# Kernel tuning notes

Measured on AMD Instinct MI355X. Metric: run time of the kernel, lower is better.

The kernel has to match this reference:

```python
import jax, jax.numpy as jnp
import numpy as np

D_MODEL = 1024
D_FF = 4096
N_HEADS = 16
D_HEAD = D_MODEL // N_HEADS
CHUNK = 64
N_HASHES = 2
N_BUCKETS = 32
EPS = 1e-5


def layer_norm(x, g, b):
    mu = jnp.mean(x, axis=-1, keepdims=True)
    var = jnp.mean(jnp.square(x - mu), axis=-1, keepdims=True)
    return (x - mu) / jnp.sqrt(var + EPS) * g + b


def look_one_back(a):
    # a: [B, H, n_chunks, chunk, ...]; concat each chunk with its predecessor
    prev = jnp.roll(a, 1, axis=2)
    return jnp.concatenate([a, prev], axis=3)


def lsh_attention(x, mask, Wqk, Wv, Wo, rot):
    # x: [B, T, D]; mask: [B, T] bool (True = valid token); shared-QK LSH attention
    B, T, D = x.shape
    H, dh, nh, nb = N_HEADS, D_HEAD, N_HASHES, N_BUCKETS
    qk = (x @ Wqk).reshape(B, T, H, dh).transpose(0, 2, 1, 3)  # [B,H,T,dh]
    v = (x @ Wv).reshape(B, T, H, dh).transpose(0, 2, 1, 3)

    # --- hashing: random rotations, argmax over +/- projections ---
    rotated = jnp.einsum('bhtd,dnr->bhtnr', qk, rot)            # [B,H,T,nh,nb/2]
    rotated = jnp.concatenate([rotated, -rotated], axis=-1)     # [B,H,T,nh,nb]
    buckets = jnp.argmax(rotated, axis=-1)                      # [B,H,T,nh]
    buckets = buckets + jnp.arange(nh) * nb                     # disjoint ids per round
    buckets = buckets.transpose(0, 1, 3, 2).reshape(B, H, nh * T)

    # --- stable bucket sort ---
    total = nh * T
    pos = jnp.arange(total) % T
    sort_key = buckets * T + pos
    sticker = jnp.argsort(sort_key, axis=-1)                    # [B,H,total]
    undo = jnp.argsort(sticker, axis=-1)
    st = sticker % T                                            # original positions

    gather = lambda a: jnp.take_along_axis(a, st[..., None], axis=2)
    sqk = gather(qk)                                            # [B,H,total,dh]
    sv = gather(v)
    smask = jnp.take_along_axis(jnp.broadcast_to(mask[:, None, :], (B, H, T)), st, axis=2)

    # --- chunked local attention with one look-back chunk ---
    nch = total // CHUNK
    bq = sqk.reshape(B, H, nch, CHUNK, dh)
    bk = bq / (jnp.linalg.norm(bq, axis=-1, keepdims=True) + 1e-9)  # shared-QK: normalized keys
    bv = sv.reshape(B, H, nch, CHUNK, dh)
    bt = st.reshape(B, H, nch, CHUNK)
    bm = smask.reshape(B, H, nch, CHUNK)

    bk2 = look_one_back(bk)                                     # [B,H,nch,2*CHUNK,dh]
    bv2 = look_one_back(bv)
    bt2 = look_one_back(bt)
    bm2 = look_one_back(bm)

    dots = jnp.einsum('bhcie,bhcje->bhcij', bq, bk2) * (dh ** -0.5)
    self_mask = bt[..., :, None] == bt2[..., None, :]           # token vs itself (soft mask)
    dots = jnp.where(self_mask, -1e5, dots)
    dots = jnp.where(bm2[..., None, :], dots, -1e9)             # padding keys

    lse = jax.nn.logsumexp(dots, axis=-1, keepdims=True)
    probs = jnp.exp(dots - lse)
    bo = jnp.einsum('bhcij,bhcje->bhcie', probs, bv2)

    # --- unsort and combine hash rounds by logsumexp weights ---
    so = bo.reshape(B, H, total, dh)
    slog = lse.reshape(B, H, total, 1)
    o = jnp.take_along_axis(so, undo[..., None], axis=2).reshape(B, H, nh, T, dh)
    logits = jnp.take_along_axis(slog, undo[..., None], axis=2).reshape(B, H, nh, T, 1)
    w = jax.nn.softmax(logits, axis=2)
    out = jnp.sum(o * w, axis=2)                                # [B,H,T,dh]
    out = out.transpose(0, 2, 1, 3).reshape(B, T, D)
    return out @ Wo


def setup_inputs() -> dict:
    key = jax.random.key(0)
    ks = jax.random.split(key, 10)
    B, T = 2, 2048
    s = 0.02
    return {
        'x': jax.random.normal(ks[0], (B, T, D_MODEL), jnp.float32),
        'attn_mask': jnp.ones((B, T), bool),
        'ln1_g': jnp.ones((D_MODEL,), jnp.float32),
        'ln1_b': jnp.zeros((D_MODEL,), jnp.float32),
        'ln2_g': jnp.ones((D_MODEL,), jnp.float32),
        'ln2_b': jnp.zeros((D_MODEL,), jnp.float32),
        'Wqk': jax.random.normal(ks[1], (D_MODEL, D_MODEL), jnp.float32) * s,
        'Wv': jax.random.normal(ks[2], (D_MODEL, D_MODEL), jnp.float32) * s,
        'Wo': jax.random.normal(ks[3], (D_MODEL, D_MODEL), jnp.float32) * s,
        'rot': jax.random.normal(ks[4], (D_HEAD, N_HASHES, N_BUCKETS // 2), jnp.float32),
        'W1': jax.random.normal(ks[5], (D_MODEL, D_FF), jnp.float32) * s,
        'b1': jnp.zeros((D_FF,), jnp.float32),
        'W2': jax.random.normal(ks[6], (D_FF, D_MODEL), jnp.float32) * s,
        'b2': jnp.zeros((D_MODEL,), jnp.float32),
    }


def reference(x, attn_mask, ln1_g, ln1_b, ln2_g, ln2_b, Wqk, Wv, Wo, rot, W1, b1, W2, b2):
    # pre-norm -> LSH self-attention -> residual
    q = layer_norm(x, ln1_g, ln1_b)
    x = x + lsh_attention(q, attn_mask, Wqk, Wv, Wo, rot)
    # pre-norm -> FFN (linear-relu-linear) -> residual
    h = layer_norm(x, ln2_g, ln2_b)
    f = jax.nn.relu(h @ W1 + b1) @ W2 + b2
    return x + f
```

## Files before the change

kernel.cpp:

```cpp
#include <hip/hip_runtime.h>

typedef unsigned short u16;
typedef unsigned int u32;
typedef unsigned long long u64;
typedef __attribute__((ext_vector_type(8))) __bf16 bf16x8;
typedef __attribute__((ext_vector_type(8))) _Float16 f16x8;
typedef __attribute__((ext_vector_type(4))) float f32x4;

#define DEVI __device__ __forceinline__

DEVI float bf2f(u16 u) { u32 x = ((u32)u) << 16; return __uint_as_float(x); }
DEVI u16 f2bf(float f) {
  u32 u = __float_as_uint(f);
  return (u16)((u + 0x7FFFu + ((u >> 16) & 1u)) >> 16);
}
DEVI u16 h_bits(_Float16 h) { return __builtin_bit_cast(u16, h); }
DEVI void gload_lds16(const void* g, void* l) {
  __builtin_amdgcn_global_load_lds((const __attribute__((address_space(1))) void*)g,
                                   (__attribute__((address_space(3))) void*)l, 16, 0, 0);
}
DEVI void swz_block(int& bx, int& by) {
  int gx = gridDim.x;
  int nwg = gx * gridDim.y;
  int wg = blockIdx.y * gx + blockIdx.x;
  int q = nwg >> 3, rr = nwg & 7, xcd = wg & 7, idx = wg >> 3;
  int s = (xcd < rr ? xcd * (q + 1) : rr * (q + 1) + (xcd - rr) * q) + idx;
  bx = s % gx;
  by = s / gx;
}

__global__ __launch_bounds__(256) void transpose_k(const float* __restrict__ in,
                                                   u16* __restrict__ out, int R, int C) {
  __shared__ float tile[32][33];
  int c0 = blockIdx.x * 32, r0 = blockIdx.y * 32;
  int tx = threadIdx.x, ty = threadIdx.y;
#pragma unroll
  for (int k = 0; k < 4; k++)
    tile[ty + 8 * k][tx] = in[(size_t)(r0 + ty + 8 * k) * C + c0 + tx];
  __syncthreads();
#pragma unroll
  for (int k = 0; k < 4; k++) {
    float v = tile[tx][ty + 8 * k];
    out[(size_t)(c0 + ty + 8 * k) * R + r0 + tx] = f2bf(v);
  }
}

__global__ __launch_bounds__(256) void ln_kernel(const float* __restrict__ x,
                                                 const float* __restrict__ g,
                                                 const float* __restrict__ b,
                                                 u16* __restrict__ obf,
                                                 u16* __restrict__ oh,
                                                 u16* __restrict__ ol) {
  int row = blockIdx.x;
  const float* xr = x + (size_t)row * 1024;
  float vals[4];
  float s = 0.f, s2 = 0.f;
#pragma unroll
  for (int i = 0; i < 4; i++) {
    float v = xr[threadIdx.x + i * 256];
    vals[i] = v; s += v; s2 += v * v;
  }
#pragma unroll
  for (int off = 32; off > 0; off >>= 1) {
    s += __shfl_down(s, off);
    s2 += __shfl_down(s2, off);
  }
  __shared__ float red[8];
  int wid = threadIdx.x >> 6;
  if ((threadIdx.x & 63) == 0) { red[wid] = s; red[4 + wid] = s2; }
  __syncthreads();
  if (threadIdx.x == 0) {
    float a = red[0] + red[1] + red[2] + red[3];
    float a2 = red[4] + red[5] + red[6] + red[7];
    float mu = a * (1.0f / 1024.0f);
    red[0] = mu;
    red[1] = a2 * (1.0f / 1024.0f) - mu * mu;
  }
  __syncthreads();
  float mu = red[0];
  float inv = 1.0f / sqrtf(red[1] + 1e-5f);
#pragma unroll
  for (int i = 0; i < 4; i++) {
    int c = threadIdx.x + i * 256;
    float y = (vals[i] - mu) * inv * g[c] + b[c];
    if (obf) obf[(size_t)row * 1024 + c] = f2bf(y);
    if (oh) {
      _Float16 hh = (_Float16)y;
      _Float16 ll = (_Float16)(y - (float)hh);
      oh[(size_t)row * 1024 + c] = h_bits(hh);
      ol[(size_t)row * 1024 + c] = h_bits(ll);
    }
  }
}

__global__ __launch_bounds__(256) void w2r_kernel(const float* __restrict__ wqk,
                                                  const float* __restrict__ rot,
                                                  u16* __restrict__ w2rh,
                                                  u16* __restrict__ w2rl) {
  int idx = blockIdx.x * 256 + threadIdx.x;
  int n = idx >> 10, c = idx & 1023;
  int h = n >> 5, rj = n & 31;
  const float* wp = wqk + (size_t)c * 1024 + h * 64;
  double acc = 0.0;
  for (int d = 0; d < 64; d++) acc += (double)wp[d] * (double)rot[d * 32 + rj];
  _Float16 hh = (_Float16)acc;
  _Float16 ll = (_Float16)(acc - (double)hh);
  w2rh[idx] = h_bits(hh);
  w2rl[idx] = h_bits(ll);
}

__global__ __launch_bounds__(256) void gemm_rot_split(const u16* __restrict__ Ah,
                                                      const u16* __restrict__ Al,
                                                      const u16* __restrict__ Bh,
                                                      const u16* __restrict__ Bl,
                                                      float* __restrict__ C) {
  __shared__ __align__(16) u16 Ash[128 * 32];
  __shared__ __align__(16) u16 Asl[128 * 32];
  __shared__ __align__(16) u16 Bsh[64 * 32];
  __shared__ __align__(16) u16 Bsl[64 * 32];
  int tid = threadIdx.x;
  int bx, by;
  swz_block(bx, by);
  int m0 = by * 128, n0 = bx * 64;
  int w = tid >> 6, l = tid & 63, lr = l & 15, g = l >> 4;
  int wm = w >> 1, wn = w & 1;
  f32x4 acc[4][2];
#pragma unroll
  for (int i = 0; i < 4; i++)
#pragma unroll
    for (int j = 0; j < 2; j++) { f32x4 z = {0.f, 0.f, 0.f, 0.f}; acc[i][j] = z; }
  for (int k0 = 0; k0 < 1024; k0 += 32) {
    __syncthreads();
#pragma unroll
    for (int e = 0; e < 2; e++) {
      int idx = e * 256 + tid;
      const u16* ga = Ah + (size_t)(m0 + (idx >> 2)) * 1024 + k0 + (idx & 3) * 8;
      gload_lds16(ga, &Ash[(e * 256 + w * 64) * 8]);
      const u16* gl = Al + (size_t)(m0 + (idx >> 2)) * 1024 + k0 + (idx & 3) * 8;
      gload_lds16(gl, &Asl[(e * 256 + w * 64) * 8]);
    }
    {
      const u16* gb = Bh + (size_t)(n0 + (tid >> 2)) * 1024 + k0 + (tid & 3) * 8;
      gload_lds16(gb, &Bsh[(w * 64) * 8]);
      const u16* gb2 = Bl + (size_t)(n0 + (tid >> 2)) * 1024 + k0 + (tid & 3) * 8;
      gload_lds16(gb2, &Bsl[(w * 64) * 8]);
    }
    __syncthreads();
    f16x8 ah[4], al[4], bh[2], bl[2];
#pragma unroll
    for (int mt = 0; mt < 4; mt++) {
      ah[mt] = *(const f16x8*)&Ash[(wm * 64 + mt * 16 + lr) * 32 + g * 8];
      al[mt] = *(const f16x8*)&Asl[(wm * 64 + mt * 16 + lr) * 32 + g * 8];
    }
#pragma unroll
    for (int nt = 0; nt < 2; nt++) {
      bh[nt] = *(const f16x8*)&Bsh[(wn * 32 + nt * 16 + lr) * 32 + g * 8];
      bl[nt] = *(const f16x8*)&Bsl[(wn * 32 + nt * 16 + lr) * 32 + g * 8];
    }
#pragma unroll
    for (int mt = 0; mt < 4; mt++)
#pragma unroll
      for (int nt = 0; nt < 2; nt++) {
        acc[mt][nt] = __builtin_amdgcn_mfma_f32_16x16x32_f16(ah[mt], bh[nt], acc[mt][nt], 0, 0, 0);
        acc[mt][nt] = __builtin_amdgcn_mfma_f32_16x16x32_f16(ah[mt], bl[nt], acc[mt][nt], 0, 0, 0);
        acc[mt][nt] = __builtin_amdgcn_mfma_f32_16x16x32_f16(al[mt], bh[nt], acc[mt][nt], 0, 0, 0);
      }
  }
#pragma unroll
  for (int mt = 0; mt < 4; mt++)
#pragma unroll
    for (int nt = 0; nt < 2; nt++)
#pragma unroll
      for (int r = 0; r < 4; r++) {
        int row = m0 + wm * 64 + mt * 16 + g * 4 + r;
        int col = n0 + wn * 32 + nt * 16 + lr;
        C[(size_t)row * 512 + col] = acc[mt][nt][r];
      }
}

__global__ __launch_bounds__(256) void bucket_kernel(const float* __restrict__ rotated,
                                                     int* __restrict__ buckets) {
  int gid = blockIdx.x * 256 + threadIdx.x;
  int bh = gid >> 12;
  int rem = gid & 4095;
  int r = rem >> 11, t = rem & 2047;
  int b = bh >> 4, h = bh & 15;
  const float* rp = rotated + (size_t)(b * 2048 + t) * 512 + h * 32 + r * 16;
  float v16[16];
#pragma unroll
  for (int j = 0; j < 16; j++) v16[j] = rp[j];
  float bv = v16[0];
  int bi = 0;
#pragma unroll
  for (int jj = 1; jj < 32; jj++) {
    float v = (jj < 16) ? v16[jj] : -v16[jj - 16];
    if (v > bv) { bv = v; bi = jj; }
  }
  buckets[bh * 4096 + r * 2048 + t] = bi + r * 32;
}

__global__ __launch_bounds__(256) void sort_kernel(const int* __restrict__ buckets,
                                                   int* __restrict__ st,
                                                   int* __restrict__ undo) {
  int bh = blockIdx.x;
  __shared__ unsigned char bk[4096];
  __shared__ unsigned char rnk[4096];
  __shared__ int cnt[64 * 64];
  __shared__ int base[64];
  int tid = threadIdx.x;
  int w = tid >> 6, lane = tid & 63;
  for (int i = tid; i < 4096; i += 256) bk[i] = (unsigned char)buckets[bh * 4096 + i];
  for (int i = tid; i < 4096; i += 256) cnt[i] = 0;
  __syncthreads();
  u64 lmask = (lane == 63) ? 0x7FFFFFFFFFFFFFFFull : ((1ull << lane) - 1ull);
#pragma unroll
  for (int it = 0; it < 16; ++it) {
    int c = w * 16 + it;
    int i = c * 64 + lane;
    int b = bk[i];
    u64 m = ~0ull;
#pragma unroll
    for (int k = 0; k < 6; k++) {
      u64 bal = __ballot((b >> k) & 1);
      m &= ((b >> k) & 1) ? bal : ~bal;
    }
    int r = __popcll(m & lmask);
    rnk[i] = (unsigned char)r;
    if (r == 0) cnt[c * 64 + b] = __popcll(m);
  }
  __syncthreads();
  if (tid < 64) {
    int acc = 0;
    for (int c = 0; c < 64; c++) {
      int t = cnt[c * 64 + tid];
      cnt[c * 64 + tid] = acc;
      acc += t;
    }
    base[tid] = acc;
  }
  __syncthreads();
  if (tid == 0) {
    int acc = 0;
    for (int b = 0; b < 64; b++) { int t = base[b]; base[b] = acc; acc += t; }
  }
  __syncthreads();
#pragma unroll
  for (int it = 0; it < 16; ++it) {
    int c = w * 16 + it;
    int i = c * 64 + lane;
    int b = bk[i];
    int pos = base[b] + cnt[c * 64 + b] + rnk[i];
    st[bh * 4096 + pos] = i & 2047;
    undo[bh * 4096 + i] = pos;
  }
}

__global__ __launch_bounds__(256) void attn_kernel(const u16* __restrict__ qkv,
                                                   const int* __restrict__ st,
                                                   u16* __restrict__ so,
                                                   float* __restrict__ slog) {
  const int c = blockIdx.x;
  const int bh = blockIdx.y;
  const int b = bh >> 4, h = bh & 15;
  __shared__ __align__(16) u16 Q[64 * 72];
  __shared__ __align__(16) u16 Kl[128 * 72];
  __shared__ __align__(16) u16 Vt[64 * 136];
  __shared__ __align__(16) u16 P[64 * 136];
  __shared__ int bts[128];
  int tid = threadIdx.x;
  {
    int j = tid >> 1, half = tid & 1;
    int cc = (j < 64) ? c : ((c + 63) & 63);
    int t = st[bh * 4096 + cc * 64 + (j & 63)];
    size_t base = ((size_t)(b * 2048 + t)) * 2048 + h * 64 + half * 32;
    __align__(16) u16 raw[32];
    *(uint4*)(&raw[0]) = *(const uint4*)(qkv + base);
    *(uint4*)(&raw[8]) = *(const uint4*)(qkv + base + 8);
    *(uint4*)(&raw[16]) = *(const uint4*)(qkv + base + 16);
    *(uint4*)(&raw[24]) = *(const uint4*)(qkv + base + 24);
    float fv[32];
    float ss = 0.f;
#pragma unroll
    for (int e = 0; e < 32; e++) { fv[e] = bf2f(raw[e]); ss += fv[e] * fv[e]; }
    ss += __shfl_xor(ss, 1);
    float scale = 1.0f / (sqrtf(ss) + 1e-9f);
#pragma unroll
    for (int e = 0; e < 32; e++) Kl[j * 72 + half * 32 + e] = f2bf(fv[e] * scale);
    if (j < 64) {
#pragma unroll
      for (int e = 0; e < 32; e++) Q[j * 72 + half * 32 + e] = raw[e];
    }
    if (half == 0) bts[j] = t;
    __align__(16) u16 vr[32];
    *(uint4*)(&vr[0]) = *(const uint4*)(qkv + base + 1024);
    *(uint4*)(&vr[8]) = *(const uint4*)(qkv + base + 1032);
    *(uint4*)(&vr[16]) = *(const uint4*)(qkv + base + 1040);
    *(uint4*)(&vr[24]) = *(const uint4*)(qkv + base + 1048);
#pragma unroll
    for (int e = 0; e < 32; e++) Vt[(half * 32 + e) * 136 + j] = vr[e];
  }
  __syncthreads();
  int w = tid >> 6, l = tid & 63;
  int lr = l & 15, g = l >> 4;
  bf16x8 aq0 = *(const bf16x8*)&Q[(w * 16 + lr) * 72 + g * 8];
  bf16x8 aq1 = *(const bf16x8*)&Q[(w * 16 + lr) * 72 + 32 + g * 8];
  float dd[8][4];
#pragma unroll
  for (int n = 0; n < 8; n++) {
    f32x4 acc = {0.f, 0.f, 0.f, 0.f};
    bf16x8 b0 = *(const bf16x8*)&Kl[(n * 16 + lr) * 72 + g * 8];
    acc = __builtin_amdgcn_mfma_f32_16x16x32_bf16(aq0, b0, acc, 0, 0, 0);
    bf16x8 b1 = *(const bf16x8*)&Kl[(n * 16 + lr) * 72 + 32 + g * 8];
    acc = __builtin_amdgcn_mfma_f32_16x16x32_bf16(aq1, b1, acc, 0, 0, 0);
#pragma unroll
    for (int r = 0; r < 4; r++) dd[n][r] = acc[r];
  }
  int btq[4];
#pragma unroll
  for (int r = 0; r < 4; r++) btq[r] = bts[w * 16 + g * 4 + r];
  float mrow[4] = {-3e38f, -3e38f, -3e38f, -3e38f};
#pragma unroll
  for (int n = 0; n < 8; n++) {
    int btk = bts[n * 16 + lr];
#pragma unroll
    for (int r = 0; r < 4; r++) {
      float v = dd[n][r] * 0.125f;
      if (btq[r] == btk) v = -1e5f;
      dd[n][r] = v;
      mrow[r] = fmaxf(mrow[r], v);
    }
  }
#pragma unroll
  for (int off = 1; off < 16; off <<= 1)
#pragma unroll
    for (int r = 0; r < 4; r++) mrow[r] = fmaxf(mrow[r], __shfl_xor(mrow[r], off));
  float se[4] = {0.f, 0.f, 0.f, 0.f};
#pragma unroll
  for (int n = 0; n < 8; n++)
#pragma unroll
    for (int r = 0; r < 4; r++) se[r] += expf(dd[n][r] - mrow[r]);
#pragma unroll
  for (int off = 1; off < 16; off <<= 1)
#pragma unroll
    for (int r = 0; r < 4; r++) se[r] += __shfl_xor(se[r], off);
  float lse[4];
#pragma unroll
  for (int r = 0; r < 4; r++) lse[r] = mrow[r] + logf(se[r]);
#pragma unroll
  for (int n = 0; n < 8; n++)
#pragma unroll
    for (int r = 0; r < 4; r++) {
      float p = expf(dd[n][r] - lse[r]);
      P[(w * 16 + g * 4 + r) * 136 + n * 16 + lr] = f2bf(p);
    }
  if (lr == 0) {
#pragma unroll
    for (int r = 0; r < 4; r++)
      slog[bh * 4096 + c * 64 + w * 16 + g * 4 + r] = lse[r];
  }
  __syncthreads();
  f32x4 o[4];
#pragma unroll
  for (int n2 = 0; n2 < 4; n2++) { f32x4 z = {0.f, 0.f, 0.f, 0.f}; o[n2] = z; }
#pragma unroll
  for (int ks = 0; ks < 4; ks++) {
    bf16x8 ap = *(const bf16x8*)&P[(w * 16 + lr) * 136 + ks * 32 + g * 8];
#pragma unroll
    for (int n2 = 0; n2 < 4; n2++) {
      bf16x8 bv = *(const bf16x8*)&Vt[(n2 * 16 + lr) * 136 + ks * 32 + g * 8];
      o[n2] = __builtin_amdgcn_mfma_f32_16x16x32_bf16(ap, bv, o[n2], 0, 0, 0);
    }
  }
#pragma unroll
  for (int n2 = 0; n2 < 4; n2++)
#pragma unroll
    for (int r = 0; r < 4; r++)
      so[((size_t)bh * 4096 + c * 64 + w * 16 + g * 4 + r) * 64 + n2 * 16 + lr] =
          f2bf(o[n2][r]);
}

__global__ __launch_bounds__(256) void combine_kernel(const u16* __restrict__ so,
                                                      const float* __restrict__ slog,
                                                      const int* __restrict__ undo,
                                                      u16* __restrict__ attn_comb) {
  int bh = blockIdx.y;
  int b = bh >> 4, h = bh & 15;
  int t = blockIdx.x * 4 + (threadIdx.x >> 6);
  int d = threadIdx.x & 63;
  int j0 = undo[bh * 4096 + t];
  int j1 = undo[bh * 4096 + 2048 + t];
  float l0 = slog[bh * 4096 + j0], l1 = slog[bh * 4096 + j1];
  float m = fmaxf(l0, l1);
  float e0 = expf(l0 - m), e1 = expf(l1 - m);
  float inv = 1.0f / (e0 + e1);
  float o = (e0 * inv) * bf2f(so[((size_t)bh * 4096 + j0) * 64 + d]) +
            (e1 * inv) * bf2f(so[((size_t)bh * 4096 + j1) * 64 + d]);
  attn_comb[((size_t)(b * 2048 + t)) * 1024 + h * 64 + d] = f2bf(o);
}

template <int EPI>
__global__ __launch_bounds__(256) void gemm_bf16(const u16* __restrict__ A,
                                                 const u16* __restrict__ Bt,
                                                 void* __restrict__ Cv,
                                                 const float* __restrict__ bias,
                                                 const float* __restrict__ resid,
                                                 int M, int N, int K) {
  __shared__ __align__(16) u16 As[2][128 * 32];
  __shared__ __align__(16) u16 Bs[2][128 * 32];
  int tid = threadIdx.x;
  int bx, by;
  swz_block(bx, by);
  int m0 = by * 128, n0 = bx * 128;
  int w = tid >> 6, l = tid & 63, lr = l & 15, g = l >> 4;
  int wm = w >> 1, wn = w & 1;
  int sw = lr & 3;
  f32x4 acc[4][4];
#pragma unroll
  for (int i = 0; i < 4; i++)
#pragma unroll
    for (int j = 0; j < 4; j++) { f32x4 z = {0.f, 0.f, 0.f, 0.f}; acc[i][j] = z; }

  auto stage = [&](int buf, int k0) {
#pragma unroll
    for (int e = 0; e < 2; e++) {
      int idx = e * 256 + tid;
      int row = idx >> 2;
      int slot = (idx & 3) ^ (row & 3);
      gload_lds16(A + (size_t)(m0 + row) * K + k0 + slot * 8,
                  &As[buf][(e * 256 + w * 64) * 8]);
      gload_lds16(Bt + (size_t)(n0 + row) * K + k0 + slot * 8,
                  &Bs[buf][(e * 256 + w * 64) * 8]);
    }
  };

  const int NT = K >> 5;
  stage(0, 0);
  asm volatile("s_waitcnt vmcnt(0)" ::: "memory");
  __builtin_amdgcn_s_barrier();
  for (int t = 0; t < NT; ++t) {
    int cur = t & 1;
    if (t + 1 < NT) stage(cur ^ 1, (t + 1) << 5);
    bf16x8 af[4], bfr[4];
#pragma unroll
    for (int mt = 0; mt < 4; mt++)
      af[mt] = *(const bf16x8*)&As[cur][(wm * 64 + mt * 16 + lr) * 32 + (g ^ sw) * 8];
#pragma unroll
    for (int nt = 0; nt < 4; nt++)
      bfr[nt] = *(const bf16x8*)&Bs[cur][(wn * 64 + nt * 16 + lr) * 32 + (g ^ sw) * 8];
#pragma unroll
    for (int mt = 0; mt < 4; mt++)
#pragma unroll
      for (int nt = 0; nt < 4; nt++)
        acc[mt][nt] =
            __builtin_amdgcn_mfma_f32_16x16x32_bf16(af[mt], bfr[nt], acc[mt][nt], 0, 0, 0);
    asm volatile("s_waitcnt vmcnt(0)" ::: "memory");
    __builtin_amdgcn_s_barrier();
  }
#pragma unroll
  for (int mt = 0; mt < 4; mt++)
#pragma unroll
    for (int nt = 0; nt < 4; nt++)
#pragma unroll
      for (int r = 0; r < 4; r++) {
        int row = m0 + wm * 64 + mt * 16 + g * 4 + r;
        int col = n0 + wn * 64 + nt * 16 + lr;
        float v = acc[mt][nt][r];
        if constexpr (EPI == 1) {
          v += resid[(size_t)row * N + col];
          ((float*)Cv)[(size_t)row * N + col] = v;
        } else if constexpr (EPI == 2) {
          v += bias[col];
          v = fmaxf(v, 0.f);
          ((u16*)Cv)[(size_t)row * N + col] = f2bf(v);
        } else if constexpr (EPI == 3) {
          v += bias[col] + resid[(size_t)row * N + col];
          ((float*)Cv)[(size_t)row * N + col] = v;
        } else {
          ((u16*)Cv)[(size_t)row * N + col] = f2bf(v);
        }
      }
}

template <int EPI>
__global__ __launch_bounds__(256) void gemm_bf16_n64(const u16* __restrict__ A,
                                                     const u16* __restrict__ Bt,
                                                     void* __restrict__ Cv,
                                                     const float* __restrict__ bias,
                                                     const float* __restrict__ resid,
                                                     int M, int N, int K) {
  __shared__ __align__(16) u16 As[2][128 * 64];
  __shared__ __align__(16) u16 Bs[2][64 * 64];
  int tid = threadIdx.x;
  int bx, by;
  swz_block(bx, by);
  int m0 = by * 128, n0 = bx * 64;
  int w = tid >> 6, l = tid & 63, lr = l & 15, g = l >> 4;
  int swa = lr & 7;
  f32x4 acc[2][4];
#pragma unroll
  for (int i = 0; i < 2; i++)
#pragma unroll
    for (int j = 0; j < 4; j++) { f32x4 z = {0.f, 0.f, 0.f, 0.f}; acc[i][j] = z; }

  auto stage = [&](int buf, int k0) {
#pragma unroll
    for (int e = 0; e < 4; e++) {
      int idx = e * 256 + tid;
      int row = idx >> 3, s = idx & 7;
      gload_lds16(A + (size_t)(m0 + row) * K + k0 + ((s ^ (row & 7)) * 8),
                  &As[buf][(e * 256 + w * 64) * 8]);
    }
#pragma unroll
    for (int e = 0; e < 2; e++) {
      int idx = e * 256 + tid;
      int row = idx >> 3, s = idx & 7;
      gload_lds16(Bt + (size_t)(n0 + row) * K + k0 + ((s ^ (row & 7)) * 8),
                  &Bs[buf][(e * 256 + w * 64) * 8]);
    }
  };

  const int NT = K >> 6;
  stage(0, 0);
  asm volatile("s_waitcnt vmcnt(0)" ::: "memory");
  __builtin_amdgcn_s_barrier();
  for (int t = 0; t < NT; ++t) {
    int cur = t & 1;
    if (t + 1 < NT) stage(cur ^ 1, (t + 1) << 6);
    bf16x8 af[2][2], bfr[4][2];
#pragma unroll
    for (int mt = 0; mt < 2; mt++)
#pragma unroll
      for (int ks = 0; ks < 2; ks++)
        af[mt][ks] = *(const bf16x8*)&As[cur][(w * 32 + mt * 16 + lr) * 64 +
                                             (((ks * 4 + g) ^ swa) * 8)];
#pragma unroll
    for (int nt = 0; nt < 4; nt++)
#pragma unroll
      for (int ks = 0; ks < 2; ks++)
        bfr[nt][ks] = *(const bf16x8*)&Bs[cur][(nt * 16 + lr) * 64 +
                                              (((ks * 4 + g) ^ swa) * 8)];
#pragma unroll
    for (int ks = 0; ks < 2; ks++)
#pragma unroll
      for (int mt = 0; mt < 2; mt++)
#pragma unroll
        for (int nt = 0; nt < 4; nt++)
          acc[mt][nt] = __builtin_amdgcn_mfma_f32_16x16x32_bf16(af[mt][ks], bfr[nt][ks],
                                                                acc[mt][nt], 0, 0, 0);
    asm volatile("s_waitcnt vmcnt(0)" ::: "memory");
    __builtin_amdgcn_s_barrier();
  }
#pragma unroll
  for (int mt = 0; mt < 2; mt++)
#pragma unroll
    for (int nt = 0; nt < 4; nt++)
#pragma unroll
      for (int r = 0; r < 4; r++) {
        int row = m0 + w * 32 + mt * 16 + g * 4 + r;
        int col = n0 + nt * 16 + lr;
        float v = acc[mt][nt][r];
        if constexpr (EPI == 1) {
          v += resid[(size_t)row * N + col];
          ((float*)Cv)[(size_t)row * N + col] = v;
        } else if constexpr (EPI == 2) {
          v += bias[col];
          v = fmaxf(v, 0.f);
          ((u16*)Cv)[(size_t)row * N + col] = f2bf(v);
        } else if constexpr (EPI == 3) {
          v += bias[col] + resid[(size_t)row * N + col];
          ((float*)Cv)[(size_t)row * N + col] = v;
        } else {
          ((u16*)Cv)[(size_t)row * N + col] = f2bf(v);
        }
      }
}

#define BARR __builtin_amdgcn_s_barrier()
#define LOAD_A_Q(curv, qmv)                                                         \
  {                                                                                 \
    _Pragma("unroll") for (int mf = 0; mf < 4; mf++) {                              \
      _Pragma("unroll") for (int ks = 0; ks < 2; ks++) {                            \
        int row_ = wm * 128 + (qmv)*64 + mf * 16 + lr;                              \
        a[mf][ks] = *(const bf16x8*)&Al[curv][row_ * 64 +                           \
                                              (((ks * 4 + g) ^ (lr & 7)) * 8)];     \
      }                                                                             \
    }                                                                               \
  }
#define LOAD_B_Q(curv, qnv)                                                         \
  {                                                                                 \
    _Pragma("unroll") for (int nf = 0; nf < 2; nf++) {                              \
      _Pragma("unroll") for (int ks = 0; ks < 2; ks++) {                            \
        int row_ = wn * 64 + (qnv)*32 + nf * 16 + lr;                               \
        bfr[nf][ks] = *(const bf16x8*)&Bl[curv][row_ * 64 +                         \
                                                (((ks * 4 + g) ^ (lr & 7)) * 8)];   \
      }                                                                             \
    }                                                                               \
  }
#define MFMA_Q(QM, QN)                                                              \
  {                                                                                 \
    _Pragma("unroll") for (int ks = 0; ks < 2; ks++) {                              \
      _Pragma("unroll") for (int mf = 0; mf < 4; mf++) {                            \
        _Pragma("unroll") for (int nf = 0; nf < 2; nf++) {                          \
          acc[(QM)*4 + mf][(QN)*2 + nf] = __builtin_amdgcn_mfma_f32_16x16x32_bf16(  \
              a[mf][ks], bfr[nf][ks], acc[(QM)*4 + mf][(QN)*2 + nf], 0, 0, 0);      \
        }                                                                           \
      }                                                                             \
    }                                                                               \
  }

template <int EPI>
__global__ __launch_bounds__(512, 2) void gemm_bf16_256(const u16* __restrict__ A,
                                                        const u16* __restrict__ Bt,
                                                        void* __restrict__ Cv,
                                                        const float* __restrict__ bias,
                                                        const float* __restrict__ resid,
                                                        int M, int N, int K) {
  __shared__ __align__(16) u16 Al[2][256 * 64];
  __shared__ __align__(16) u16 Bl[2][256 * 64];
  int tid = threadIdx.x;
  int bx, by;
  swz_block(bx, by);
  int m0 = by * 256, n0 = bx * 256;
  int w = tid >> 6, l = tid & 63, lr = l & 15, g = l >> 4;
  int wm = w >> 2, wn = w & 3;
  f32x4 acc[8][4];
#pragma unroll
  for (int i = 0; i < 8; i++)
#pragma unroll
    for (int j = 0; j < 4; j++) { f32x4 z = {0.f, 0.f, 0.f, 0.f}; acc[i][j] = z; }

  auto stage_unit = [&](int u, int buf, int k0) {
#pragma unroll
    for (int j = 0; j < 2; j++) {
      int r = j * 64 + (tid >> 3);
      int s = tid & 7;
      int co = (s ^ (r & 7)) * 8;
      int r0 = j * 64 + (w << 3);
      const u16* src;
      u16* dst;
      if (u == 0) {
        int row = (r < 64) ? r : r + 64;
        int row0 = (r0 < 64) ? r0 : r0 + 64;
        src = A + (size_t)(m0 + row) * K + k0 + co;
        dst = &Al[buf][row0 * 64];
      } else if (u == 2) {
        int row = (r < 64) ? r + 64 : r + 128;
        int row0 = (r0 < 64) ? r0 + 64 : r0 + 128;
        src = A + (size_t)(m0 + row) * K + k0 + co;
        dst = &Al[buf][row0 * 64];
      } else if (u == 1) {
        int row = ((r >> 5) << 6) + (r & 31);
        int row0 = ((r0 >> 5) << 6) + (r0 & 31);
        src = Bt + (size_t)(n0 + row) * K + k0 + co;
        dst = &Bl[buf][row0 * 64];
      } else {
        int row = ((r >> 5) << 6) + 32 + (r & 31);
        int row0 = ((r0 >> 5) << 6) + 32 + (r0 & 31);
        src = Bt + (size_t)(n0 + row) * K + k0 + co;
        dst = &Bl[buf][row0 * 64];
      }
      gload_lds16(src, dst);
    }
  };

  bf16x8 a[4][2], bfr[2][2];
  const int NT = K >> 6;
  stage_unit(0, 0, 0);
  stage_unit(1, 0, 0);
  stage_unit(2, 0, 0);
  stage_unit(3, 0, 0);
  asm volatile("s_waitcnt vmcnt(0)" ::: "memory");
  BARR;
  for (int t = 0; t < NT; ++t) {
    int cur = t & 1, nxt = cur ^ 1;
    int k1 = (t + 1) << 6;
    if (t + 1 < NT) {
      stage_unit(0, nxt, k1);
      stage_unit(1, nxt, k1);
      stage_unit(2, nxt, k1);
      stage_unit(3, nxt, k1);
    }
    LOAD_A_Q(cur, 0);
    LOAD_B_Q(cur, 0);
    MFMA_Q(0, 0);
    LOAD_A_Q(cur, 1);
    MFMA_Q(1, 0);
    LOAD_B_Q(cur, 1);
    MFMA_Q(1, 1);
    LOAD_A_Q(cur, 0);
    MFMA_Q(0, 1);
    asm volatile("s_waitcnt vmcnt(0)" ::: "memory");
    BARR;
  }
#pragma unroll
  for (int mf = 0; mf < 8; mf++)
#pragma unroll
    for (int nf = 0; nf < 4; nf++)
#pragma unroll
      for (int r = 0; r < 4; r++) {
        int row = m0 + wm * 128 + mf * 16 + g * 4 + r;
        int col = n0 + wn * 64 + nf * 16 + lr;
        float v = acc[mf][nf][r];
        if constexpr (EPI == 1) {
          v += resid[(size_t)row * N + col];
          ((float*)Cv)[(size_t)row * N + col] = v;
        } else if constexpr (EPI == 2) {
          v += bias[col];
          v = fmaxf(v, 0.f);
          ((u16*)Cv)[(size_t)row * N + col] = f2bf(v);
        } else if constexpr (EPI == 3) {
          v += bias[col] + resid[(size_t)row * N + col];
          ((float*)Cv)[(size_t)row * N + col] = v;
        } else {
          ((u16*)Cv)[(size_t)row * N + col] = f2bf(v);
        }
      }
}

extern "C" void kernel_launch(void* const* d_in, const int* in_sizes, int n_in,
                              void* d_out, int out_size, void* d_ws, size_t ws_size,
                              hipStream_t stream) {
  (void)in_sizes; (void)n_in; (void)out_size; (void)ws_size;
  const float* x    = (const float*)d_in[0];
  const float* ln1g = (const float*)d_in[2];
  const float* ln1b = (const float*)d_in[3];
  const float* ln2g = (const float*)d_in[4];
  const float* ln2b = (const float*)d_in[5];
  const float* Wqk  = (const float*)d_in[6];
  const float* Wv   = (const float*)d_in[7];
  const float* Wo   = (const float*)d_in[8];
  const float* rot  = (const float*)d_in[9];
  const float* W1   = (const float*)d_in[10];
  const float* b1   = (const float*)d_in[11];
  const float* W2   = (const float*)d_in[12];
  const float* b2   = (const float*)d_in[13];

  char* ws = (char*)d_ws;
  size_t off = 0;
  auto alloc = [&](size_t n) { size_t r = off; off += (n + 255) & ~(size_t)255; return r; };
  float* xn_f32  = (float*)(ws + alloc(4096ull * 1024 * 4));
  u16*   xn_bf   = (u16*)(ws + alloc(4096ull * 1024 * 2));
  u16*   wqkv_t  = (u16*)(ws + alloc(2048ull * 1024 * 2));
  u16*   wo_t    = (u16*)(ws + alloc(1024ull * 1024 * 2));
  u16*   w1_t    = (u16*)(ws + alloc(4096ull * 1024 * 2));
  u16*   w2_t    = (u16*)(ws + alloc(4096ull * 1024 * 2));
  size_t qk_off  = alloc(4096ull * 2048 * 2);
  u16*   qkvb    = (u16*)(ws + qk_off);
  float* w2r     = (float*)(ws + alloc(1024ull * 512 * 4));
  float* rotated = (float*)(ws + alloc(4096ull * 512 * 4));
  int*   buckets = (int*)(ws + alloc(32ull * 4096 * 4));
  int*   stp     = (int*)(ws + alloc(32ull * 4096 * 4));
  int*   undo    = (int*)(ws + alloc(32ull * 4096 * 4));
  u16*   so      = (u16*)(ws + alloc(32ull * 4096 * 64 * 2));
  float* slog    = (float*)(ws + alloc(32ull * 4096 * 4));
  u16*   xn_h   = (u16*)xn_f32;
  u16*   xn_l   = xn_h + 4096ull * 1024;
  float* x_attn = xn_f32;
  u16*   h2     = xn_bf;
  u16*   w2r_h  = (u16*)w2r;
  u16*   w2r_l  = w2r_h + 512ull * 1024;
  u16*   attn_comb = (u16*)rotated;
  u16*   f1 = (u16*)(ws + qk_off);

  dim3 tb(32, 8);
  transpose_k<<<dim3(32, 32), tb, 0, stream>>>(Wqk, wqkv_t, 1024, 1024);
  transpose_k<<<dim3(32, 32), tb, 0, stream>>>(Wv, wqkv_t + 1024ull * 1024, 1024, 1024);
  transpose_k<<<dim3(32, 32), tb, 0, stream>>>(Wo, wo_t, 1024, 1024);
  transpose_k<<<dim3(128, 32), tb, 0, stream>>>(W1, w1_t, 1024, 4096);
  transpose_k<<<dim3(32, 128), tb, 0, stream>>>(W2, w2_t, 4096, 1024);

  ln_kernel<<<4096, 256, 0, stream>>>(x, ln1g, ln1b, xn_bf, xn_h, xn_l);

  gemm_bf16<0><<<dim3(16, 32), 256, 0, stream>>>(xn_bf, wqkv_t, qkvb, nullptr, nullptr,
                                                 4096, 2048, 1024);

  w2r_kernel<<<2048, 256, 0, stream>>>(Wqk, rot, w2r_h, w2r_l);
  gemm_rot_split<<<dim3(8, 32), 256, 0, stream>>>(xn_h, xn_l, w2r_h, w2r_l, rotated);
  bucket_kernel<<<512, 256, 0, stream>>>(rotated, buckets);
  sort_kernel<<<32, 256, 0, stream>>>(buckets, stp, undo);
  attn_kernel<<<dim3(64, 32), 256, 0, stream>>>(qkvb, stp, so, slog);
  combine_kernel<<<dim3(512, 32), 256, 0, stream>>>(so, slog, undo, attn_comb);

  gemm_bf16_n64<1><<<dim3(16, 32), 256, 0, stream>>>(attn_comb, wo_t, x_attn, nullptr, x,
                                                     4096, 1024, 1024);
  ln_kernel<<<4096, 256, 0, stream>>>(x_attn, ln2g, ln2b, h2, nullptr, nullptr);
  gemm_bf16_256<2><<<dim3(16, 16), 512, 0, stream>>>(h2, w1_t, f1, b1, nullptr,
                                                     4096, 4096, 1024);
  gemm_bf16_n64<3><<<dim3(16, 32), 256, 0, stream>>>(f1, w2_t, (float*)d_out, b2, x_attn,
                                                     4096, 1024, 4096);
}
```

Before: 280.3 us.

## Split-K the final FFN down-projection GEMM with a separate reduce kernel

The W2 GEMM (M=4096, N=1024, K=4096) now runs with the K dimension split across two z-slices, doubling the block count from 512 to 1024 so more CUs stay busy. Each slice writes fp32 partials to a new workspace buffer. A vectorised reduce kernel then sums the two partials and adds the bias and residual. This costs extra global traffic (two 16MB partial writes plus reads) and one more launch, and it only takes effect if the workspace is large enough.

```diff
diff --git a/kernel.cpp b/kernel.cpp
--- a/kernel.cpp
+++ b/kernel.cpp
@@ -481,7 +481,7 @@
       }
 }
 
-template <int EPI>
+template <int EPI, int SPLITK = 0>
 __global__ __launch_bounds__(256) void gemm_bf16_n64(const u16* __restrict__ A,
                                                      const u16* __restrict__ Bt,
                                                      void* __restrict__ Cv,
@@ -494,6 +494,11 @@
   int bx, by;
   swz_block(bx, by);
   int m0 = by * 128, n0 = bx * 64;
+  int kbase = 0, klen = K;
+  if constexpr (SPLITK == 1) {
+    klen = K >> 1;
+    kbase = blockIdx.z * klen;
+  }
   int w = tid >> 6, l = tid & 63, lr = l & 15, g = l >> 4;
   int swa = lr & 7;
   f32x4 acc[2][4];
@@ -507,19 +512,19 @@
     for (int e = 0; e < 4; e++) {
       int idx = e * 256 + tid;
       int row = idx >> 3, s = idx & 7;
-      gload_lds16(A + (size_t)(m0 + row) * K + k0 + ((s ^ (row & 7)) * 8),
+      gload_lds16(A + (size_t)(m0 + row) * K + kbase + k0 + ((s ^ (row & 7)) * 8),
                   &As[buf][(e * 256 + w * 64) * 8]);
     }
 #pragma unroll
     for (int e = 0; e < 2; e++) {
       int idx = e * 256 + tid;
       int row = idx >> 3, s = idx & 7;
-      gload_lds16(Bt + (size_t)(n0 + row) * K + k0 + ((s ^ (row & 7)) * 8),
+      gload_lds16(Bt + (size_t)(n0 + row) * K + kbase + k0 + ((s ^ (row & 7)) * 8),
                   &Bs[buf][(e * 256 + w * 64) * 8]);
     }
   };
 
-  const int NT = K >> 6;
+  const int NT = klen >> 6;
   stage(0, 0);
   asm volatile("s_waitcnt vmcnt(0)" ::: "memory");
   __builtin_amdgcn_s_barrier();
@@ -550,6 +555,8 @@
     asm volatile("s_waitcnt vmcnt(0)" ::: "memory");
     __builtin_amdgcn_s_barrier();
   }
+  float* pout = (float*)Cv;
+  if constexpr (SPLITK == 1) pout += (size_t)blockIdx.z * M * N;
 #pragma unroll
   for (int mt = 0; mt < 2; mt++)
 #pragma unroll
@@ -559,7 +566,9 @@
         int row = m0 + w * 32 + mt * 16 + g * 4 + r;
         int col = n0 + nt * 16 + lr;
         float v = acc[mt][nt][r];
-        if constexpr (EPI == 1) {
+        if constexpr (SPLITK == 1) {
+          pout[(size_t)row * N + col] = v;
+        } else if constexpr (EPI == 1) {
           v += resid[(size_t)row * N + col];
           ((float*)Cv)[(size_t)row * N + col] = v;
         } else if constexpr (EPI == 2) {
@@ -573,6 +582,25 @@
           ((u16*)Cv)[(size_t)row * N + col] = f2bf(v);
         }
       }
+}
+
+__global__ __launch_bounds__(256) void splitk_reduce(const float* __restrict__ p0,
+                                                     const float* __restrict__ p1,
+                                                     const float* __restrict__ bias,
+                                                     const float* __restrict__ resid,
+                                                     float* __restrict__ out) {
+  int i4 = blockIdx.x * 256 + threadIdx.x;
+  int colb = (i4 << 2) & 1023;
+  float4 a = ((const float4*)p0)[i4];
+  float4 b = ((const float4*)p1)[i4];
+  float4 rr = ((const float4*)resid)[i4];
+  float4 bb = *(const float4*)(bias + colb);
+  float4 o;
+  o.x = a.x + b.x + bb.x + rr.x;
+  o.y = a.y + b.y + bb.y + rr.y;
+  o.z = a.z + b.z + bb.z + rr.z;
+  o.w = a.w + b.w + bb.w + rr.w;
+  ((float4*)out)[i4] = o;
 }
 
 #define BARR __builtin_amdgcn_s_barrier()
@@ -720,7 +748,7 @@
 extern "C" void kernel_launch(void* const* d_in, const int* in_sizes, int n_in,
                               void* d_out, int out_size, void* d_ws, size_t ws_size,
                               hipStream_t stream) {
-  (void)in_sizes; (void)n_in; (void)out_size; (void)ws_size;
+  (void)in_sizes; (void)n_in; (void)out_size;
   const float* x    = (const float*)d_in[0];
   const float* ln1g = (const float*)d_in[2];
   const float* ln1b = (const float*)d_in[3];
@@ -753,6 +781,9 @@
   int*   undo    = (int*)(ws + alloc(32ull * 4096 * 4));
   u16*   so      = (u16*)(ws + alloc(32ull * 4096 * 64 * 2));
   float* slog    = (float*)(ws + alloc(32ull * 4096 * 4));
+  size_t skp_off = alloc(2ull * 4096 * 1024 * 4);
+  float* skp     = (float*)(ws + skp_off);
+  bool use_splitk = (ws_size >= off);
   u16*   xn_h   = (u16*)xn_f32;
   u16*   xn_l   = xn_h + 4096ull * 1024;
   float* x_attn = xn_f32;
@@ -786,6 +817,13 @@
   ln_kernel<<<4096, 256, 0, stream>>>(x_attn, ln2g, ln2b, h2, nullptr, nullptr);
   gemm_bf16_256<2><<<dim3(16, 16), 512, 0, stream>>>(h2, w1_t, f1, b1, nullptr,
                                                      4096, 4096, 1024);
-  gemm_bf16_n64<3><<<dim3(16, 32), 256, 0, stream>>>(f1, w2_t, (float*)d_out, b2, x_attn,
-                                                     4096, 1024, 4096);
-}
+  if (use_splitk) {
+    gemm_bf16_n64<0, 1><<<dim3(16, 32, 2), 256, 0, stream>>>(f1, w2_t, skp, nullptr,
+                                                             nullptr, 4096, 1024, 4096);
+    splitk_reduce<<<4096, 256, 0, stream>>>(skp, skp + 4096ull * 1024, b2, x_attn,
+                                            (float*)d_out);
+  } else {
+    gemm_bf16_n64<3><<<dim3(16, 32), 256, 0, stream>>>(f1, w2_t, (float*)d_out, b2,
+                                                       x_attn, 4096, 1024, 4096);
+  }
+}
```

Result: slower. 293.0 us (+4.5%).
